# Optimization experiments

Hardware: AMD Instinct MI355X
Metric: run time of the kernel (lower is better)

## Reference

```python
import jax, jax.numpy as jnp
import numpy as np

N_GRAPHS = 4
NODES_PER_GRAPH = 8192
N_NODES = N_GRAPHS * NODES_PER_GRAPH
N_EDGES = N_NODES * 16
IN_DIM = 3
HID = 128
K_OUT = 512
MAX_WAVELENGTH = 10000.0


def _glorot(k, shape):
    lim = (6.0 / (shape[0] + shape[1])) ** 0.5
    return jax.random.uniform(k, shape, jnp.float32, -lim, lim)


def setup_inputs() -> dict:
    key = jax.random.key(0)
    ks = jax.random.split(key, 12)
    z = lambda *s: jnp.zeros(s, jnp.float32)
    return {
        "x": jax.random.normal(ks[0], (N_NODES, IN_DIM), jnp.float32),
        "mesh_pos": jax.random.uniform(ks[1], (N_NODES, 2), jnp.float32),
        "mesh_edges": jax.random.randint(ks[2], (N_EDGES, 2), 0, N_NODES, jnp.int32),
        "batch_idx": jnp.arange(N_NODES, dtype=jnp.int32) // NODES_PER_GRAPH,
        "proj_w": _glorot(ks[3], (IN_DIM, HID)), "proj_b": z(HID),
        "msg_w1": _glorot(ks[4], (2 * HID, HID)), "msg_b1": z(HID),
        "msg_w2": _glorot(ks[5], (HID, HID)), "msg_b2": z(HID),
        "upd_w1": _glorot(ks[6], (2 * HID, HID)), "upd_b1": z(HID),
        "upd_w2": _glorot(ks[7], (HID, HID)), "upd_b2": z(HID),
        "pool_rel_w": _glorot(ks[8], (HID, 1)), "pool_rel_b": z(1),
        "pool_root_w": _glorot(ks[9], (HID, 1)),
    }


def _sincos_embed(pos):
    # ContinuousSincosEmbed: HID=128, ndim=2 -> 64 channels per coord dim, 32 freqs
    dim_per_ndim = HID // 2
    omega = 1.0 / MAX_WAVELENGTH ** (jnp.arange(0, dim_per_ndim, 2, dtype=jnp.float32) / dim_per_ndim)
    ang = pos[:, :, None] * omega  # [N, ndim, 32]
    emb = jnp.concatenate([jnp.sin(ang), jnp.cos(ang)], axis=-1)  # [N, ndim, 64]
    return emb.reshape(pos.shape[0], HID)


def reference(x, mesh_pos, mesh_edges, batch_idx, proj_w, proj_b,
              msg_w1, msg_b1, msg_w2, msg_b2, upd_w1, upd_b1, upd_w2, upd_b2,
              pool_rel_w, pool_rel_b, pool_root_w):
    src, dst = mesh_edges[:, 0], mesh_edges[:, 1]  # edge_index[0]=j(src), [1]=i(dst)
    h = x @ proj_w + proj_b + _sincos_embed(mesh_pos)
    cnt = jnp.maximum(jax.ops.segment_sum(jnp.ones((N_EDGES,), h.dtype), dst, num_segments=N_NODES), 1.0)
    # message passing layer (depth=1): message MLP on [x_i, x_j], scatter-mean, residual update MLP
    m_in = jnp.concatenate([h[dst], h[src]], axis=-1)  # [E, 2H]
    m = jax.nn.silu(m_in @ msg_w1 + msg_b1) @ msg_w2 + msg_b2
    agg = jax.ops.segment_sum(m, dst, num_segments=N_NODES) / cnt[:, None]
    h = h + (jax.nn.silu(jnp.concatenate([h, agg], axis=-1) @ upd_w1 + upd_b1) @ upd_w2 + upd_b2)
    # SAGPooling score: GraphConv(HID,1,aggr='mean'), tanh nonlinearity
    nagg = jax.ops.segment_sum(h[src], dst, num_segments=N_NODES) / cnt[:, None]
    score = jnp.tanh((nagg @ pool_rel_w + pool_rel_b + h @ pool_root_w)[:, 0])
    # fixed top-k per graph (batch_idx is contiguous blocks of NODES_PER_GRAPH)
    topv, topi = jax.lax.top_k(score.reshape(N_GRAPHS, NODES_PER_GRAPH), K_OUT)
    perm = (topi + jnp.arange(N_GRAPHS, dtype=topi.dtype)[:, None] * NODES_PER_GRAPH).reshape(-1)
    x_pool = h[perm] * topv.reshape(-1)[:, None]
    batch_pool = jnp.repeat(jnp.arange(N_GRAPHS, dtype=batch_idx.dtype), K_OUT)
    return x_pool, batch_pool
```

## Files before the change

### kernel.cpp

```cpp
#include <hip/hip_runtime.h>
#include <hip/hip_bf16.h>
#include <math.h>

#define N_NODESC 32768
#define N_EDGESC 524288
#define NPG 8192
#define KOUT 512

typedef unsigned short u16;
typedef unsigned int u32;
typedef unsigned long long u64;

__device__ __forceinline__ float siluf(float x) {
    return x / (1.f + __expf(-x));
}

__global__ __launch_bounds__(256) void k_h0(const float* __restrict__ x,
                                            const float* __restrict__ pos,
                                            const float* __restrict__ pw,
                                            const float* __restrict__ pb,
                                            float* __restrict__ h,
                                            int* __restrict__ deg) {
    int gid = blockIdx.x * 256 + threadIdx.x;
    if (gid < N_NODESC) deg[gid] = 0;
    int node = blockIdx.x * 2 + (threadIdx.x >> 7);
    int c = threadIdx.x & 127;
    float x0 = x[node * 3 + 0];
    float x1 = x[node * 3 + 1];
    float x2 = x[node * 3 + 2];
    float acc = x0 * pw[c] + x1 * pw[128 + c] + x2 * pw[256 + c];
    acc += pb[c];
    int dim = c >> 6;
    int inner = c & 63;
    int jj = inner & 31;
    float p = pos[node * 2 + dim];
    float omega = exp2f(-(float)jj * 0.41524101186092027f);
    float ang = p * omega;
    acc += (inner < 32) ? __sinf(ang) : __cosf(ang);
    h[(size_t)node * 128 + c] = acc;
}

__global__ __launch_bounds__(256) void k_deg(const int* __restrict__ edges, int* __restrict__ deg) {
    int e = blockIdx.x * 256 + threadIdx.x;
    if (e < N_EDGESC) {
        int2 e2 = ((const int2*)edges)[e];
        atomicAdd(&deg[e2.y], 1);
    }
}

__global__ __launch_bounds__(1024) void k_scan(const int* __restrict__ deg,
                                               int* __restrict__ off, int* __restrict__ cur,
                                               float* __restrict__ rs, float* __restrict__ bg) {
    __shared__ int ls[1024];
    int tid = threadIdx.x;
    int base = tid * 32;
    int v[32];
    int s = 0;
#pragma unroll
    for (int j = 0; j < 32; j++) { v[j] = deg[base + j]; s += v[j]; }
    ls[tid] = s;
    __syncthreads();
    for (int ofs = 1; ofs < 1024; ofs <<= 1) {
        int t = (tid >= ofs) ? ls[tid - ofs] : 0;
        __syncthreads();
        ls[tid] += t;
        __syncthreads();
    }
    int run = ls[tid] - s;
#pragma unroll
    for (int j = 0; j < 32; j++) {
        off[base + j] = run;
        cur[base + j] = run;
        int d = v[j];
        rs[base + j] = 1.f / (float)(d > 0 ? d : 1);
        bg[base + j] = d > 0 ? 1.f : 0.f;
        run += d;
    }
}

__global__ __launch_bounds__(256) void k_fill(const int* __restrict__ edges,
                                              int* __restrict__ cur, int* __restrict__ csr) {
    int e = blockIdx.x * 256 + threadIdx.x;
    if (e < N_EDGESC) {
        int2 e2 = ((const int2*)edges)[e];
        int pos = atomicAdd(&cur[e2.y], 1);
        csr[pos] = e2.x;
    }
}

__global__ __launch_bounds__(256) void gemm_dual(const float* __restrict__ A,
                                                 const float* __restrict__ Wv,
                                                 const float* __restrict__ Wu,
                                                 const float* __restrict__ bu,
                                                 float* __restrict__ V, float* __restrict__ U) {
    int cg = threadIdx.x & 31;
    int rg = threadIdx.x >> 5;
    int m0 = blockIdx.x * 32 + rg * 4;
    int c0 = cg * 4;
    float av[4][4], au[4][4];
#pragma unroll
    for (int r = 0; r < 4; r++)
#pragma unroll
        for (int c = 0; c < 4; c++) { av[r][c] = 0.f; au[r][c] = 0.f; }

    const float* Arow = A + (size_t)m0 * 128;
    for (int k0 = 0; k0 < 128; k0 += 4) {
        float4 a[4];
#pragma unroll
        for (int r = 0; r < 4; r++) a[r] = *(const float4*)(Arow + r * 128 + k0);
#pragma unroll
        for (int kk = 0; kk < 4; kk++) {
            float4 wv = *(const float4*)(Wv + (size_t)(k0 + kk) * 128 + c0);
            float4 wu = *(const float4*)(Wu + (size_t)(k0 + kk) * 128 + c0);
#pragma unroll
            for (int r = 0; r < 4; r++) {
                float aa = ((const float*)&a[r])[kk];
                av[r][0] += aa * wv.x; av[r][1] += aa * wv.y; av[r][2] += aa * wv.z; av[r][3] += aa * wv.w;
                au[r][0] += aa * wu.x; au[r][1] += aa * wu.y; au[r][2] += aa * wu.z; au[r][3] += aa * wu.w;
            }
        }
    }
#pragma unroll
    for (int r = 0; r < 4; r++) {
        int row = m0 + r;
        float4 ov, ou;
        ov.x = av[r][0]; ov.y = av[r][1]; ov.z = av[r][2]; ov.w = av[r][3];
        ou.x = au[r][0] + bu[c0]; ou.y = au[r][1] + bu[c0 + 1];
        ou.z = au[r][2] + bu[c0 + 2]; ou.w = au[r][3] + bu[c0 + 3];
        *(float4*)(V + (size_t)row * 128 + c0) = ov;
        *(float4*)(U + (size_t)row * 128 + c0) = ou;
    }
}

__global__ __launch_bounds__(256) void gemm128(const float* __restrict__ A1, const float* __restrict__ W1,
                                               const float* __restrict__ A2, const float* __restrict__ W2,
                                               const float* __restrict__ bias,
                                               const float* __restrict__ rs, const float* __restrict__ bg,
                                               const float* __restrict__ resid,
                                               float* __restrict__ C, int act,
                                               const float* __restrict__ wrel, const float* __restrict__ wroot,
                                               float* __restrict__ pout, float* __restrict__ rout) {
    int cg = threadIdx.x & 31;
    int rg = threadIdx.x >> 5;
    int m0 = blockIdx.x * 32 + rg * 4;
    int c0 = cg * 4;
    float acc[4][4];
#pragma unroll
    for (int r = 0; r < 4; r++)
#pragma unroll
        for (int c = 0; c < 4; c++) acc[r][c] = 0.f;

    const float* Arow1 = A1 + (size_t)m0 * 128;
    const float* Arow2 = A2 ? (A2 + (size_t)m0 * 128) : nullptr;

    for (int k0 = 0; k0 < 128; k0 += 4) {
        float4 a1[4];
#pragma unroll
        for (int r = 0; r < 4; r++) a1[r] = *(const float4*)(Arow1 + r * 128 + k0);
#pragma unroll
        for (int kk = 0; kk < 4; kk++) {
            float4 w = *(const float4*)(W1 + (size_t)(k0 + kk) * 128 + c0);
#pragma unroll
            for (int r = 0; r < 4; r++) {
                float a = ((const float*)&a1[r])[kk];
                acc[r][0] += a * w.x;
                acc[r][1] += a * w.y;
                acc[r][2] += a * w.z;
                acc[r][3] += a * w.w;
            }
        }
        if (A2) {
            float4 a2[4];
#pragma unroll
            for (int r = 0; r < 4; r++) a2[r] = *(const float4*)(Arow2 + r * 128 + k0);
#pragma unroll
            for (int kk = 0; kk < 4; kk++) {
                float4 w = *(const float4*)(W2 + (size_t)(k0 + kk) * 128 + c0);
#pragma unroll
                for (int r = 0; r < 4; r++) {
                    float a = ((const float*)&a2[r])[kk];
                    acc[r][0] += a * w.x;
                    acc[r][1] += a * w.y;
                    acc[r][2] += a * w.z;
                    acc[r][3] += a * w.w;
                }
            }
        }
    }

    float prel[4], prot[4];
#pragma unroll
    for (int r = 0; r < 4; r++) {
        int row = m0 + r;
        float rsv = rs ? rs[row] : 1.f;
        float bgv = bg ? bg[row] : 1.f;
        float4 o;
        float* op = (float*)&o;
#pragma unroll
        for (int c = 0; c < 4; c++) {
            float xv = acc[r][c] * rsv;
            if (bias) xv += bias[c0 + c] * bgv;
            if (resid) xv += resid[(size_t)row * 128 + c0 + c];
            if (act) xv = siluf(xv);
            op[c] = xv;
        }
        if (wrel) {
            prel[r] = op[0] * wrel[c0] + op[1] * wrel[c0 + 1] + op[2] * wrel[c0 + 2] + op[3] * wrel[c0 + 3];
            prot[r] = op[0] * wroot[c0] + op[1] * wroot[c0 + 1] + op[2] * wroot[c0 + 2] + op[3] * wroot[c0 + 3];
        }
        *(float4*)(C + (size_t)row * 128 + c0) = o;
    }
    if (wrel) {
#pragma unroll
        for (int r = 0; r < 4; r++) {
            float a = prel[r], b = prot[r];
#pragma unroll
            for (int m = 1; m < 32; m <<= 1) {
                a += __shfl_xor(a, m);
                b += __shfl_xor(b, m);
            }
            if (cg == 0) { pout[m0 + r] = a; rout[m0 + r] = b; }
        }
    }
}

__global__ __launch_bounds__(256) void k_accum_S(const float* __restrict__ v,
                                                 const int* __restrict__ csr, const int* __restrict__ off,
                                                 const int* __restrict__ deg, float* S) {
    int d = blockIdx.x * 4 + (threadIdx.x >> 6);
    int lane = threadIdx.x & 63;
    float* srow = S + (size_t)d * 128;
    float u0 = srow[lane];
    float u1 = srow[64 + lane];
    float a0 = 0.f, a1 = 0.f;
    int o = off[d], n = deg[d];
    for (int base = 0; base < n; base += 64) {
        int cnt = min(64, n - base);
        int sall = (lane < cnt) ? csr[o + base + lane] : 0;
        int s0 = __shfl(sall, 0);
        float p00 = v[(size_t)s0 * 128 + lane];
        float p01 = v[(size_t)s0 * 128 + 64 + lane];
        float p10 = 0.f, p11 = 0.f;
        if (cnt > 1) {
            int s1 = __shfl(sall, 1);
            p10 = v[(size_t)s1 * 128 + lane];
            p11 = v[(size_t)s1 * 128 + 64 + lane];
        }
        for (int j = 0; j < cnt; j++) {
            float cv0 = p00, cv1 = p01;
            p00 = p10; p01 = p11;
            if (j + 2 < cnt) {
                int sn = __shfl(sall, j + 2);
                p10 = v[(size_t)sn * 128 + lane];
                p11 = v[(size_t)sn * 128 + 64 + lane];
            }
            a0 += siluf(u0 + cv0);
            a1 += siluf(u1 + cv1);
        }
    }
    srow[lane] = a0;
    srow[64 + lane] = a1;
}

__global__ __launch_bounds__(256) void k_score(const float* __restrict__ p, const float* __restrict__ r,
                                               const int* __restrict__ csr, const int* __restrict__ off,
                                               const int* __restrict__ deg, const float* __restrict__ relb,
                                               float* __restrict__ score) {
    int d = blockIdx.x * 4 + (threadIdx.x >> 6);
    int lane = threadIdx.x & 63;
    int o = off[d], n = deg[d];
    float a = 0.f;
    for (int j = lane; j < n; j += 64) a += p[csr[o + j]];
    for (int m = 32; m > 0; m >>= 1) a += __shfl_xor(a, m);
    if (lane == 0) {
        float cnt = (float)(n > 0 ? n : 1);
        score[d] = tanhf(a / cnt + relb[0] + r[d]);
    }
}

__global__ __launch_bounds__(1024) void k_topk(const float* __restrict__ score, const float* __restrict__ h,
                                               float* __restrict__ out) {
    __shared__ u32 ms[NPG];
    __shared__ u32 hist[256];
    __shared__ u32 sbuf[1024];
    __shared__ u64 sel[KOUT];
    __shared__ float ordv[KOUT];
    __shared__ int ordi[KOUT];
    __shared__ u32 selCnt, sPrefix, sNeed, sB;

    int g = blockIdx.x;
    int tid = threadIdx.x;

    for (int i = tid; i < NPG; i += 1024) {
        u32 u = __float_as_uint(score[(size_t)g * NPG + i]);
        ms[i] = (u & 0x80000000u) ? ~u : (u | 0x80000000u);
    }
    if (tid == 0) { sNeed = KOUT; sPrefix = 0; selCnt = 0; }
    __syncthreads();

    for (int pass = 0; pass < 4; pass++) {
        int shift = 24 - pass * 8;
        if (tid < 256) hist[tid] = 0;
        __syncthreads();
        u32 pfx = sPrefix;
        for (int i = tid; i < NPG; i += 1024) {
            u32 v = ms[i];
            if (pass == 0 || (v >> (shift + 8)) == pfx)
                atomicAdd(&hist[(v >> shift) & 255u], 1u);
        }
        __syncthreads();
        if (tid < 256) sbuf[tid] = hist[tid];
        __syncthreads();
        for (int ofs = 1; ofs < 256; ofs <<= 1) {
            u32 t = 0;
            if (tid < 256 && tid + ofs < 256) t = sbuf[tid + ofs];
            __syncthreads();
            if (tid < 256) sbuf[tid] += t;
            __syncthreads();
        }
        u32 need = sNeed;
        if (tid < 256) {
            if (sbuf[tid] >= need && (tid == 255 || sbuf[tid + 1] < need)) sB = (u32)tid;
        }
        __syncthreads();
        if (tid == 0) {
            u32 B = sB;
            u32 above = (B == 255) ? 0u : sbuf[B + 1];
            sNeed = need - above;
            sPrefix = (sPrefix << 8) | B;
        }
        __syncthreads();
    }
    u32 T = sPrefix;
    u32 rTie = sNeed;

    int base = tid * 8;
    u32 lc = 0;
#pragma unroll
    for (int j = 0; j < 8; j++) lc += (ms[base + j] == T);
    __syncthreads();
    sbuf[tid] = lc;
    __syncthreads();
    u32 own = lc;
    for (int ofs = 1; ofs < 1024; ofs <<= 1) {
        u32 t = (tid >= ofs) ? sbuf[tid - ofs] : 0;
        __syncthreads();
        sbuf[tid] += t;
        __syncthreads();
    }
    u32 excl = sbuf[tid] - own;

#pragma unroll
    for (int j = 0; j < 8; j++) {
        int i = base + j;
        u32 v = ms[i];
        bool pick = (v > T) || ((v == T) && (excl < rTie));
        if (v == T) excl++;
        if (pick) {
            u32 slot = atomicAdd(&selCnt, 1u);
            sel[slot] = ((u64)v << 32) | (u32)(NPG - 1 - i);
        }
    }
    __syncthreads();

    if (tid < KOUT) {
        u64 mine = sel[tid];
        int rank = 0;
        for (int j = 0; j < KOUT; j++) rank += (sel[j] > mine);
        u32 v = (u32)(mine >> 32);
        int idx = NPG - 1 - (int)(mine & 0xFFFFFFFFu);
        u32 uu = (v & 0x80000000u) ? (v & 0x7FFFFFFFu) : ~v;
        ordv[rank] = __uint_as_float(uu);
        ordi[rank] = idx;
    }
    __syncthreads();

    for (int t = tid; t < KOUT * 128; t += 1024) {
        int r = t >> 7, c = t & 127;
        int node = g * NPG + ordi[r];
        out[((size_t)g * KOUT + r) * 128 + c] = h[(size_t)node * 128 + c] * ordv[r];
    }
    for (int t = tid; t < KOUT; t += 1024)
        out[(size_t)4 * KOUT * 128 + (size_t)g * KOUT + t] = (float)g;
}

extern "C" void kernel_launch(void* const* d_in, const int* in_sizes, int n_in,
                              void* d_out, int out_size, void* d_ws, size_t ws_size,
                              hipStream_t stream) {
    const float* x        = (const float*)d_in[0];
    const float* mesh_pos = (const float*)d_in[1];
    const int*   edges    = (const int*)d_in[2];
    const float* proj_w   = (const float*)d_in[4];
    const float* proj_b   = (const float*)d_in[5];
    const float* msg_w1   = (const float*)d_in[6];
    const float* msg_b1   = (const float*)d_in[7];
    const float* msg_w2   = (const float*)d_in[8];
    const float* msg_b2   = (const float*)d_in[9];
    const float* upd_w1   = (const float*)d_in[10];
    const float* upd_b1   = (const float*)d_in[11];
    const float* upd_w2   = (const float*)d_in[12];
    const float* upd_b2   = (const float*)d_in[13];
    const float* pool_rel_w  = (const float*)d_in[14];
    const float* pool_rel_b  = (const float*)d_in[15];
    const float* pool_root_w = (const float*)d_in[16];
    float* out = (float*)d_out;

    char* w = (char*)d_ws;
    float* h  = (float*)(w);
    float* v  = (float*)(w + (1ull << 24));
    float* S  = (float*)(w + (2ull << 24));
    char* sm  = w + (3ull << 24);
    int*   deg   = (int*)(sm);
    int*   off   = (int*)(sm + 131072);
    int*   cur   = (int*)(sm + 262144);
    float* rsA   = (float*)(sm + 393216);
    float* bgA   = (float*)(sm + 524288);
    float* pp    = (float*)(sm + 655360);
    float* rr    = (float*)(sm + 786432);
    float* score = (float*)(sm + 917504);
    int*   csr   = (int*)(sm + 1048576);

    k_h0<<<N_NODESC / 2, 256, 0, stream>>>(x, mesh_pos, proj_w, proj_b, h, deg);
    k_deg<<<N_EDGESC / 256, 256, 0, stream>>>(edges, deg);
    k_scan<<<1, 1024, 0, stream>>>(deg, off, cur, rsA, bgA);
    k_fill<<<N_EDGESC / 256, 256, 0, stream>>>(edges, cur, csr);

    gemm_dual<<<1024, 256, 0, stream>>>(h, msg_w1 + 128 * 128, msg_w1, msg_b1, v, S);
    k_accum_S<<<N_NODESC / 4, 256, 0, stream>>>(v, csr, off, deg, S);
    gemm128<<<1024, 256, 0, stream>>>(S, msg_w2, nullptr, nullptr, msg_b2,
                                      rsA, bgA, nullptr, v, 0,
                                      nullptr, nullptr, nullptr, nullptr);
    gemm128<<<1024, 256, 0, stream>>>(h, upd_w1, v, upd_w1 + 128 * 128, upd_b1,
                                      nullptr, nullptr, nullptr, S, 1,
                                      nullptr, nullptr, nullptr, nullptr);
    gemm128<<<1024, 256, 0, stream>>>(S, upd_w2, nullptr, nullptr, upd_b2,
                                      nullptr, nullptr, h, h, 0,
                                      pool_rel_w, pool_root_w, pp, rr);

    k_score<<<N_NODESC / 4, 256, 0, stream>>>(pp, rr, csr, off, deg, pool_rel_b, score);
    k_topk<<<4, 1024, 0, stream>>>(score, h, out);
}
```

Measured before the change: 451.0 us.

## Stage GEMM weights in LDS with 8-row register tiles and sort CSR neighbors

```diff
diff --git a/kernel.cpp b/kernel.cpp
--- a/kernel.cpp
+++ b/kernel.cpp
@@ -88,109 +88,111 @@
     }
 }
 
-__global__ __launch_bounds__(256) void gemm_dual(const float* __restrict__ A,
-                                                 const float* __restrict__ Wv,
-                                                 const float* __restrict__ Wu,
-                                                 const float* __restrict__ bu,
-                                                 float* __restrict__ V, float* __restrict__ U) {
-    int cg = threadIdx.x & 31;
-    int rg = threadIdx.x >> 5;
-    int m0 = blockIdx.x * 32 + rg * 4;
+__global__ __launch_bounds__(256) void k_sortcsr(int* __restrict__ csr,
+                                                 const int* __restrict__ off,
+                                                 const int* __restrict__ deg) {
+    int d = blockIdx.x * 4 + (threadIdx.x >> 6);
+    int lane = threadIdx.x & 63;
+    int o = off[d], n = deg[d];
+    if (n <= 1) return;
+    if (n <= 64) {
+        int key = (lane < n) ? csr[o + lane] : 0x7FFFFFFF;
+        for (int k = 2; k <= 64; k <<= 1) {
+            for (int j = k >> 1; j > 0; j >>= 1) {
+                int partner = __shfl_xor(key, j);
+                bool asc = ((lane & k) == 0);
+                bool keepMin = (((lane & j) == 0) == asc);
+                key = keepMin ? min(key, partner) : max(key, partner);
+            }
+        }
+        if (lane < n) csr[o + lane] = key;
+    } else {
+        if (lane == 0) {
+            for (int i = o + 1; i < o + n; i++) {
+                int x = csr[i];
+                int j = i - 1;
+                while (j >= o && csr[j] > x) { csr[j + 1] = csr[j]; j--; }
+                csr[j + 1] = x;
+            }
+        }
+    }
+}
+
+__global__ __launch_bounds__(256, 2) void gemm_lds(const float* __restrict__ A, const float* __restrict__ W,
+                                                   const float* __restrict__ bias,
+                                                   const float* __restrict__ rs, const float* __restrict__ bg,
+                                                   const float* __restrict__ resid,
+                                                   float* __restrict__ C, int act,
+                                                   const float* __restrict__ wrel, const float* __restrict__ wroot,
+                                                   float* __restrict__ pout, float* __restrict__ rout) {
+    __shared__ float Ws[128 * 128];
+    int tid = threadIdx.x;
+
+    {
+        const float4* Wg = (const float4*)W;
+        float4* Wl = (float4*)Ws;
+#pragma unroll
+        for (int i = 0; i < 16; i++) Wl[tid + i * 256] = Wg[tid + i * 256];
+    }
+    __syncthreads();
+
+    int cg = tid & 31;
+    int rg = tid >> 5;
+    int m0 = blockIdx.x * 64 + rg * 8;
     int c0 = cg * 4;
-    float av[4][4], au[4][4];
-#pragma unroll
-    for (int r = 0; r < 4; r++)
-#pragma unroll
-        for (int c = 0; c < 4; c++) { av[r][c] = 0.f; au[r][c] = 0.f; }
-
-    const float* Arow = A + (size_t)m0 * 128;
-    for (int k0 = 0; k0 < 128; k0 += 4) {
-        float4 a[4];
-#pragma unroll
-        for (int r = 0; r < 4; r++) a[r] = *(const float4*)(Arow + r * 128 + k0);
-#pragma unroll
-        for (int kk = 0; kk < 4; kk++) {
-            float4 wv = *(const float4*)(Wv + (size_t)(k0 + kk) * 128 + c0);
-            float4 wu = *(const float4*)(Wu + (size_t)(k0 + kk) * 128 + c0);
-#pragma unroll
-            for (int r = 0; r < 4; r++) {
-                float aa = ((const float*)&a[r])[kk];
-                av[r][0] += aa * wv.x; av[r][1] += aa * wv.y; av[r][2] += aa * wv.z; av[r][3] += aa * wv.w;
-                au[r][0] += aa * wu.x; au[r][1] += aa * wu.y; au[r][2] += aa * wu.z; au[r][3] += aa * wu.w;
-            }
-        }
-    }
-#pragma unroll
-    for (int r = 0; r < 4; r++) {
-        int row = m0 + r;
-        float4 ov, ou;
-        ov.x = av[r][0]; ov.y = av[r][1]; ov.z = av[r][2]; ov.w = av[r][3];
-        ou.x = au[r][0] + bu[c0]; ou.y = au[r][1] + bu[c0 + 1];
-        ou.z = au[r][2] + bu[c0 + 2]; ou.w = au[r][3] + bu[c0 + 3];
-        *(float4*)(V + (size_t)row * 128 + c0) = ov;
-        *(float4*)(U + (size_t)row * 128 + c0) = ou;
-    }
-}
-
-__global__ __launch_bounds__(256) void gemm128(const float* __restrict__ A1, const float* __restrict__ W1,
-                                               const float* __restrict__ A2, const float* __restrict__ W2,
-                                               const float* __restrict__ bias,
-                                               const float* __restrict__ rs, const float* __restrict__ bg,
-                                               const float* __restrict__ resid,
-                                               float* __restrict__ C, int act,
-                                               const float* __restrict__ wrel, const float* __restrict__ wroot,
-                                               float* __restrict__ pout, float* __restrict__ rout) {
-    int cg = threadIdx.x & 31;
-    int rg = threadIdx.x >> 5;
-    int m0 = blockIdx.x * 32 + rg * 4;
-    int c0 = cg * 4;
-    float acc[4][4];
-#pragma unroll
-    for (int r = 0; r < 4; r++)
+    const float* Ar = A + (size_t)m0 * 128;
+
+    float acc[8][4];
+#pragma unroll
+    for (int r = 0; r < 8; r++)
 #pragma unroll
         for (int c = 0; c < 4; c++) acc[r][c] = 0.f;
 
-    const float* Arow1 = A1 + (size_t)m0 * 128;
-    const float* Arow2 = A2 ? (A2 + (size_t)m0 * 128) : nullptr;
-
-    for (int k0 = 0; k0 < 128; k0 += 4) {
-        float4 a1[4];
-#pragma unroll
-        for (int r = 0; r < 4; r++) a1[r] = *(const float4*)(Arow1 + r * 128 + k0);
-#pragma unroll
-        for (int kk = 0; kk < 4; kk++) {
-            float4 w = *(const float4*)(W1 + (size_t)(k0 + kk) * 128 + c0);
-#pragma unroll
-            for (int r = 0; r < 4; r++) {
-                float a = ((const float*)&a1[r])[kk];
-                acc[r][0] += a * w.x;
-                acc[r][1] += a * w.y;
-                acc[r][2] += a * w.z;
-                acc[r][3] += a * w.w;
-            }
-        }
-        if (A2) {
-            float4 a2[4];
-#pragma unroll
-            for (int r = 0; r < 4; r++) a2[r] = *(const float4*)(Arow2 + r * 128 + k0);
-#pragma unroll
-            for (int kk = 0; kk < 4; kk++) {
-                float4 w = *(const float4*)(W2 + (size_t)(k0 + kk) * 128 + c0);
-#pragma unroll
-                for (int r = 0; r < 4; r++) {
-                    float a = ((const float*)&a2[r])[kk];
-                    acc[r][0] += a * w.x;
-                    acc[r][1] += a * w.y;
-                    acc[r][2] += a * w.z;
-                    acc[r][3] += a * w.w;
-                }
-            }
-        }
-    }
-
-    float prel[4], prot[4];
-#pragma unroll
-    for (int r = 0; r < 4; r++) {
+    float4 aA[8], aB[8], wA[4], wB[4];
+
+#define LOAD_A(buf, k)                                                   \
+    {                                                                    \
+        _Pragma("unroll") for (int r = 0; r < 8; r++)                    \
+            buf[r] = *(const float4*)(Ar + r * 128 + (k));               \
+    }
+#define LOAD_W(buf, k)                                                   \
+    {                                                                    \
+        _Pragma("unroll") for (int kk = 0; kk < 4; kk++)                 \
+            buf[kk] = *(const float4*)(Ws + ((k) + kk) * 128 + c0);      \
+    }
+#define COMPUTE(ab, wb)                                                  \
+    {                                                                    \
+        _Pragma("unroll") for (int kk = 0; kk < 4; kk++) {               \
+            float4 wv = wb[kk];                                          \
+            _Pragma("unroll") for (int r = 0; r < 8; r++) {              \
+                float a = ((const float*)&ab[r])[kk];                    \
+                acc[r][0] += a * wv.x;                                   \
+                acc[r][1] += a * wv.y;                                   \
+                acc[r][2] += a * wv.z;                                   \
+                acc[r][3] += a * wv.w;                                   \
+            }                                                            \
+        }                                                                \
+    }
+
+    LOAD_A(aA, 0)
+    LOAD_W(wA, 0)
+    for (int k0 = 0; k0 < 128; k0 += 8) {
+        LOAD_A(aB, k0 + 4)
+        LOAD_W(wB, k0 + 4)
+        COMPUTE(aA, wA)
+        if (k0 + 8 < 128) {
+            LOAD_A(aA, k0 + 8)
+            LOAD_W(wA, k0 + 8)
+        }
+        COMPUTE(aB, wB)
+    }
+#undef LOAD_A
+#undef LOAD_W
+#undef COMPUTE
+
+    float prel[8], prot[8];
+#pragma unroll
+    for (int r = 0; r < 8; r++) {
         int row = m0 + r;
         float rsv = rs ? rs[row] : 1.f;
         float bgv = bg ? bg[row] : 1.f;
@@ -198,7 +200,8 @@
         float* op = (float*)&o;
 #pragma unroll
         for (int c = 0; c < 4; c++) {
-            float xv = acc[r][c] * rsv;
+            float xv = acc[r][c];
+            xv *= rsv;
             if (bias) xv += bias[c0 + c] * bgv;
             if (resid) xv += resid[(size_t)row * 128 + c0 + c];
             if (act) xv = siluf(xv);
@@ -212,7 +215,7 @@
     }
     if (wrel) {
 #pragma unroll
-        for (int r = 0; r < 4; r++) {
+        for (int r = 0; r < 8; r++) {
             float a = prel[r], b = prot[r];
 #pragma unroll
             for (int m = 1; m < 32; m <<= 1) {
@@ -424,18 +427,21 @@
     k_deg<<<N_EDGESC / 256, 256, 0, stream>>>(edges, deg);
     k_scan<<<1, 1024, 0, stream>>>(deg, off, cur, rsA, bgA);
     k_fill<<<N_EDGESC / 256, 256, 0, stream>>>(edges, cur, csr);
-
-    gemm_dual<<<1024, 256, 0, stream>>>(h, msg_w1 + 128 * 128, msg_w1, msg_b1, v, S);
+    k_sortcsr<<<N_NODESC / 4, 256, 0, stream>>>(csr, off, deg);
+
+    gemm_lds<<<512, 256, 0, stream>>>(h, msg_w1 + 128 * 128, nullptr, nullptr, nullptr, nullptr,
+                                      v, 0, nullptr, nullptr, nullptr, nullptr);
+    gemm_lds<<<512, 256, 0, stream>>>(h, msg_w1, msg_b1, nullptr, nullptr, nullptr,
+                                      S, 0, nullptr, nullptr, nullptr, nullptr);
     k_accum_S<<<N_NODESC / 4, 256, 0, stream>>>(v, csr, off, deg, S);
-    gemm128<<<1024, 256, 0, stream>>>(S, msg_w2, nullptr, nullptr, msg_b2,
-                                      rsA, bgA, nullptr, v, 0,
-                                      nullptr, nullptr, nullptr, nullptr);
-    gemm128<<<1024, 256, 0, stream>>>(h, upd_w1, v, upd_w1 + 128 * 128, upd_b1,
-                                      nullptr, nullptr, nullptr, S, 1,
-                                      nullptr, nullptr, nullptr, nullptr);
-    gemm128<<<1024, 256, 0, stream>>>(S, upd_w2, nullptr, nullptr, upd_b2,
-                                      nullptr, nullptr, h, h, 0,
-                                      pool_rel_w, pool_root_w, pp, rr);
+    gemm_lds<<<512, 256, 0, stream>>>(S, msg_w2, msg_b2, rsA, bgA, nullptr,
+                                      v, 0, nullptr, nullptr, nullptr, nullptr);
+    gemm_lds<<<512, 256, 0, stream>>>(h, upd_w1, upd_b1, nullptr, nullptr, nullptr,
+                                      S, 0, nullptr, nullptr, nullptr, nullptr);
+    gemm_lds<<<512, 256, 0, stream>>>(v, upd_w1 + 128 * 128, nullptr, nullptr, nullptr, S,
+                                      v, 1, nullptr, nullptr, nullptr, nullptr);
+    gemm_lds<<<512, 256, 0, stream>>>(v, upd_w2, upd_b2, nullptr, nullptr, h,
+                                      h, 0, pool_rel_w, pool_root_w, pp, rr);
 
     k_score<<<N_NODESC / 4, 256, 0, stream>>>(pp, rr, csr, off, deg, pool_rel_b, score);
     k_topk<<<4, 1024, 0, stream>>>(score, h, out);
```

Result: faster. 434.3 us (-3.7%).
